# Performance work log

Hardware: AMD Instinct MI355X
Metric: run time of the kernel (lower is better)

The kernel has to match this reference:

```python
import jax, jax.numpy as jnp
import numpy as np

N_NODES = 20000
N_EDGES = 320000
F_IN = 256
HID = 256
N_CLS = 5


def _glorot(key, shape):
    lim = np.sqrt(6.0 / (shape[0] + shape[1]))
    return jax.random.uniform(key, shape, jnp.float32, -lim, lim)


def setup_inputs() -> dict:
    key = jax.random.key(0)
    ks = jax.random.split(key, 12)
    x1 = jax.random.normal(ks[0], (N_NODES, F_IN), jnp.float32)
    x2 = jax.random.normal(ks[1], (N_NODES, F_IN), jnp.float32)
    ei1 = jax.random.randint(ks[2], (2, N_EDGES), 0, N_NODES, jnp.int64 if jax.config.jax_enable_x64 else jnp.int32)
    ei2 = jax.random.randint(ks[3], (2, N_EDGES), 0, N_NODES, jnp.int64 if jax.config.jax_enable_x64 else jnp.int32)
    params = {
        'W1': _glorot(ks[4], (F_IN, HID)), 'b1': jnp.zeros((HID,), jnp.float32),
        'W2': _glorot(ks[5], (HID, HID)), 'b2': jnp.zeros((HID,), jnp.float32),
        'W3': _glorot(ks[6], (HID, HID)), 'b3': jnp.zeros((HID,), jnp.float32),
        'Wl': _glorot(ks[7], (HID, N_CLS)), 'bl': jnp.zeros((N_CLS,), jnp.float32),
    }
    return {'x1': x1, 'edge_index1': ei1, 'x2': x2, 'edge_index2': ei2, **params}


def gcn_conv(x, edge_index, W, b):
    # PyG GCNConv: add self-loops, symmetric normalization D^-1/2 (A+I) D^-1/2 (X W) + b
    N = x.shape[0]
    src, dst = edge_index[0], edge_index[1]
    deg = jax.ops.segment_sum(jnp.ones(src.shape[0], x.dtype), dst, num_segments=N) + 1.0
    dinv = jax.lax.rsqrt(deg)  # [N]
    xw = x @ W                 # [N, H]
    coef = (dinv[src] * dinv[dst])[:, None]  # per-edge norm
    agg = jax.ops.segment_sum(xw[src] * coef, dst, num_segments=N)
    agg = agg + xw * (dinv * dinv)[:, None]  # self-loop term
    return agg + b


def _branch(x, ei, W1, b1, W2, b2, W3, b3):
    # dropout is identity in eval mode
    h = jax.nn.relu(gcn_conv(x, ei, W1, b1))
    h = jax.nn.relu(gcn_conv(h, ei, W2, b2))
    return gcn_conv(h, ei, W3, b3)


def reference(x1, edge_index1, x2, edge_index2, W1, b1, W2, b2, W3, b3, Wl, bl):
    h1 = _branch(x1, edge_index1, W1, b1, W2, b2, W3, b3)
    h2 = _branch(x2, edge_index2, W1, b1, W2, b2, W3, b3)
    h = jnp.concatenate([h1, h2], axis=0)          # [2N, H]
    pooled = jnp.mean(h, axis=0, keepdims=True)    # batch is all zeros -> single mean pool
    return pooled @ Wl + bl                        # [1, num_classes]
```

## Files before the change

### kernel.cpp

```cpp
#include <hip/hip_runtime.h>
#include <hip/hip_bf16.h>

#define N_NODES 20000
#define N_EDGES 320000
#define HID 256
#define NQ 5000
#define NCHUNK 8

typedef __attribute__((ext_vector_type(8))) short bf16x8;
typedef __attribute__((ext_vector_type(4))) float f32x4;
typedef __attribute__((ext_vector_type(8))) unsigned short us8;

__device__ __forceinline__ float bf2f(ushort u) {
  union { unsigned int i; float f; } v; v.i = ((unsigned int)u) << 16; return v.f;
}
__device__ __forceinline__ ushort f2bf(float f) {
  union { float f; unsigned int i; } v; v.f = f;
  unsigned int r = v.i + 0x7FFFu + ((v.i >> 16) & 1u);
  return (ushort)(r >> 16);
}

__global__ void init_detect_kernel(int* cnt0, int* cnt1, float* t0, float* t1,
                                   const void* x1, const void* ei1, int* flags) {
  if (blockIdx.x == gridDim.x - 1) {
    __shared__ int cnt_wild, cnt_oddnz;
    if (threadIdx.x == 0) { cnt_wild = 0; cnt_oddnz = 0; }
    __syncthreads();
    const ushort* xu = (const ushort*)x1;
    int wild = 0;
#pragma unroll
    for (int k = 0; k < 4; k++) {
      ushort u = xu[threadIdx.x * 4 + k];
      int ex = (u >> 7) & 0xFF;
      if (ex >= 0x90) wild++;
    }
    if (wild) atomicAdd(&cnt_wild, wild);
    const int* ii = (const int*)ei1;
    if (ii[threadIdx.x * 2 + 1] != 0) atomicAdd(&cnt_oddnz, 1);
    __syncthreads();
    if (threadIdx.x == 0) {
      flags[0] = (cnt_wild > 64) ? 1 : 0;
      flags[1] = (cnt_oddnz < 8) ? 1 : 0;
    }
    return;
  }
  int i = blockIdx.x * blockDim.x + threadIdx.x;
  if (i < N_NODES) { cnt0[i] = 0; cnt1[i] = 0; t0[i] = 0.f; t1[i] = 0.f; }
}

__global__ __launch_bounds__(1024) void count_rank_kernel(
    const void* e0, const void* e1, int* cnt0, int* cnt1,
    int* rank0, int* rank1, const int* flags) {
  int b = blockIdx.y;
  const void* e = b ? e1 : e0;
  int* cnt = b ? cnt1 : cnt0;
  int* rank = b ? rank1 : rank0;
  int chunk = blockIdx.x >> 2;
  int lo = (blockIdx.x & 3) * NQ;
  int ebeg = chunk * (N_EDGES / NCHUNK);
  int eend = ebeg + (N_EDGES / NCHUNK);
  __shared__ int hist[NQ];
  __shared__ int base[NQ];
  for (int k = threadIdx.x; k < NQ; k += 1024) hist[k] = 0;
  __syncthreads();
  bool w64 = flags[1] != 0;
  const int* d32 = (const int*)e + N_EDGES;
  const long long* d64 = (const long long*)e + N_EDGES;
  for (int i = ebeg + threadIdx.x; i < eend; i += 1024) {
    int d = w64 ? (int)d64[i] : d32[i];
    unsigned q = (unsigned)(d - lo);
    if (q < NQ) atomicAdd(&hist[q], 1);
  }
  __syncthreads();
  for (int k = threadIdx.x; k < NQ; k += 1024) {
    base[k] = atomicAdd(&cnt[lo + k], hist[k]);
    hist[k] = 0;
  }
  __syncthreads();
  for (int i = ebeg + threadIdx.x; i < eend; i += 1024) {
    int d = w64 ? (int)d64[i] : d32[i];
    unsigned q = (unsigned)(d - lo);
    if (q < NQ) rank[i] = base[q] + atomicAdd(&hist[q], 1);
  }
}

__global__ __launch_bounds__(1024) void scan_kernel(const int* cnt0, const int* cnt1,
                                                    int* rp0, int* rp1,
                                                    float* dinv0, float* dinv1) {
  const int* cnt = blockIdx.x ? cnt1 : cnt0;
  int* rp = blockIdx.x ? rp1 : rp0;
  float* dinv = blockIdx.x ? dinv1 : dinv0;
  __shared__ int sd[1024];
  int tid = threadIdx.x;
  int base = tid * 20;
  int pref[20];
  int run = 0;
#pragma unroll
  for (int k = 0; k < 20; k++) {
    int i = base + k;
    int c = (i < N_NODES) ? cnt[i] : 0;
    if (i < N_NODES) dinv[i] = rsqrtf((float)c + 1.0f);
    run += c;
    pref[k] = run;
  }
  sd[tid] = run;
  __syncthreads();
  for (int off = 1; off < 1024; off <<= 1) {
    int v = (tid >= off) ? sd[tid - off] : 0;
    __syncthreads();
    sd[tid] += v;
    __syncthreads();
  }
  int offset = sd[tid] - run;
  if (tid == 0) rp[0] = 0;
#pragma unroll
  for (int k = 0; k < 20; k++) {
    int i = base + k;
    if (i < N_NODES) rp[i + 1] = offset + pref[k];
  }
}

__global__ __launch_bounds__(1024) void fill_kernel(
    const void* e0, const void* e1,
    const float* dinv0, const float* dinv1,
    const int* rp0, const int* rp1,
    const int* rank0, const int* rank1,
    unsigned int* eg0, unsigned int* eg1,
    float* t0, float* t1, const int* flags) {
  int b = blockIdx.y;
  const void* e = b ? e1 : e0;
  const float* dinv = b ? dinv1 : dinv0;
  bool w64 = flags[1] != 0;
  const int* s32 = (const int*)e;
  const int* d32 = (const int*)e + N_EDGES;
  const long long* s64 = (const long long*)e;
  const long long* d64 = (const long long*)e + N_EDGES;
  if (blockIdx.x < 313) {
    const int* rp = b ? rp1 : rp0;
    const int* rank = b ? rank1 : rank0;
    unsigned int* eg = b ? eg1 : eg0;
    int i = blockIdx.x * 1024 + threadIdx.x;
    if (i >= N_EDGES) return;
    int src = w64 ? (int)s64[i] : s32[i];
    int dst = w64 ? (int)d64[i] : d32[i];
    int slot = rp[dst] + rank[i];
    eg[slot] = (unsigned int)src | ((unsigned int)f2bf(dinv[src] * dinv[dst]) << 16);
    return;
  }
  float* t = b ? t1 : t0;
  int r = blockIdx.x - 313;
  int chunk = r >> 2;
  int lo = (r & 3) * NQ;
  int ebeg = chunk * (N_EDGES / NCHUNK);
  int eend = ebeg + (N_EDGES / NCHUNK);
  __shared__ float tl[NQ];
  for (int k = threadIdx.x; k < NQ; k += 1024) tl[k] = 0.f;
  __syncthreads();
  for (int i = ebeg + threadIdx.x; i < eend; i += 1024) {
    int src = w64 ? (int)s64[i] : s32[i];
    unsigned q = (unsigned)(src - lo);
    if (q < NQ) {
      int dst = w64 ? (int)d64[i] : d32[i];
      atomicAdd(&tl[q], dinv[dst]);
    }
  }
  __syncthreads();
  for (int k = threadIdx.x; k < NQ; k += 1024)
    atomicAdd(&t[lo + k], tl[k]);
}

__global__ __launch_bounds__(256) void gemm_kernel(
    const void* __restrict__ A0, const void* __restrict__ A1,
    const void* __restrict__ W,
    ushort* __restrict__ C0, ushort* __restrict__ C1,
    int maybe_f32, const int* __restrict__ flags) {
  const void* A = blockIdx.z ? A1 : A0;
  ushort* C = blockIdx.z ? C1 : C0;
  bool wf32 = flags[0] != 0;
  bool af32 = maybe_f32 && wf32;
  int m0 = blockIdx.x * 128;
  int n0 = blockIdx.y * 64;
  __shared__ ushort As[128][42];
  __shared__ ushort Bs[64][42];
  int tid = threadIdx.x;
  int wave = tid >> 6, lane = tid & 63;
  int quad = lane >> 4, r16 = lane & 15;
  f32x4 acc[2][4];
#pragma unroll
  for (int m = 0; m < 2; m++)
#pragma unroll
    for (int n = 0; n < 4; n++) acc[m][n] = (f32x4){0.f, 0.f, 0.f, 0.f};
  int la_row = tid >> 1;
  int la_c0 = (tid & 1) * 16;
  int bk = tid >> 3;
  int bn0 = (tid & 7) * 8;
  for (int k0 = 0; k0 < 256; k0 += 32) {
    int gr = m0 + la_row;
    if (af32) {
      const float* Af = (const float*)A;
      float4 v0 = {0,0,0,0}, v1 = v0, v2 = v0, v3 = v0;
      if (gr < N_NODES) {
        const float* pA = Af + gr * 256 + k0 + la_c0;
        v0 = *(const float4*)pA;       v1 = *(const float4*)(pA + 4);
        v2 = *(const float4*)(pA + 8); v3 = *(const float4*)(pA + 12);
      }
      ushort* d = &As[la_row][la_c0];
      d[0] = f2bf(v0.x); d[1] = f2bf(v0.y); d[2]  = f2bf(v0.z); d[3]  = f2bf(v0.w);
      d[4] = f2bf(v1.x); d[5] = f2bf(v1.y); d[6]  = f2bf(v1.z); d[7]  = f2bf(v1.w);
      d[8] = f2bf(v2.x); d[9] = f2bf(v2.y); d[10] = f2bf(v2.z); d[11] = f2bf(v2.w);
      d[12] = f2bf(v3.x); d[13] = f2bf(v3.y); d[14] = f2bf(v3.z); d[15] = f2bf(v3.w);
    } else {
      const ushort* Ab = (const ushort*)A;
      int4 w0 = {0,0,0,0}, w1 = w0;
      if (gr < N_NODES) {
        const ushort* pA = Ab + gr * 256 + k0 + la_c0;
        w0 = *(const int4*)pA;
        w1 = *(const int4*)(pA + 8);
      }
      *(int4*)&As[la_row][la_c0] = w0;
      *(int4*)&As[la_row][la_c0 + 8] = w1;
    }
    ushort wtmp[8];
    if (wf32) {
      const float* Wf = (const float*)W + (k0 + bk) * 256 + n0 + bn0;
      float4 u0 = *(const float4*)Wf;
      float4 u1 = *(const float4*)(Wf + 4);
      wtmp[0] = f2bf(u0.x); wtmp[1] = f2bf(u0.y); wtmp[2] = f2bf(u0.z); wtmp[3] = f2bf(u0.w);
      wtmp[4] = f2bf(u1.x); wtmp[5] = f2bf(u1.y); wtmp[6] = f2bf(u1.z); wtmp[7] = f2bf(u1.w);
    } else {
      *(int4*)wtmp = *(const int4*)((const ushort*)W + (k0 + bk) * 256 + n0 + bn0);
    }
#pragma unroll
    for (int j = 0; j < 8; j++) Bs[bn0 + j][bk] = wtmp[j];
    __syncthreads();
    bf16x8 a0 = *(const bf16x8*)&As[wave * 32 + r16][quad * 8];
    bf16x8 a1 = *(const bf16x8*)&As[wave * 32 + 16 + r16][quad * 8];
    bf16x8 bb0 = *(const bf16x8*)&Bs[r16][quad * 8];
    bf16x8 bb1 = *(const bf16x8*)&Bs[16 + r16][quad * 8];
    bf16x8 bb2 = *(const bf16x8*)&Bs[32 + r16][quad * 8];
    bf16x8 bb3 = *(const bf16x8*)&Bs[48 + r16][quad * 8];
    acc[0][0] = __builtin_amdgcn_mfma_f32_16x16x32_bf16(a0, bb0, acc[0][0], 0, 0, 0);
    acc[0][1] = __builtin_amdgcn_mfma_f32_16x16x32_bf16(a0, bb1, acc[0][1], 0, 0, 0);
    acc[0][2] = __builtin_amdgcn_mfma_f32_16x16x32_bf16(a0, bb2, acc[0][2], 0, 0, 0);
    acc[0][3] = __builtin_amdgcn_mfma_f32_16x16x32_bf16(a0, bb3, acc[0][3], 0, 0, 0);
    acc[1][0] = __builtin_amdgcn_mfma_f32_16x16x32_bf16(a1, bb0, acc[1][0], 0, 0, 0);
    acc[1][1] = __builtin_amdgcn_mfma_f32_16x16x32_bf16(a1, bb1, acc[1][1], 0, 0, 0);
    acc[1][2] = __builtin_amdgcn_mfma_f32_16x16x32_bf16(a1, bb2, acc[1][2], 0, 0, 0);
    acc[1][3] = __builtin_amdgcn_mfma_f32_16x16x32_bf16(a1, bb3, acc[1][3], 0, 0, 0);
    __syncthreads();
  }
#pragma unroll
  for (int m = 0; m < 2; m++) {
    int grb = m0 + wave * 32 + m * 16 + quad * 4;
#pragma unroll
    for (int r = 0; r < 4; r++) {
      int gr = grb + r;
      if (gr < N_NODES) {
        ushort* cp = C + gr * 256 + n0 + r16;
        cp[0]  = f2bf(acc[m][0][r]);
        cp[16] = f2bf(acc[m][1][r]);
        cp[32] = f2bf(acc[m][2][r]);
        cp[48] = f2bf(acc[m][3][r]);
      }
    }
  }
}

__global__ __launch_bounds__(256) void agg_kernel(
    const ushort* __restrict__ XW0, const ushort* __restrict__ XW1,
    const float* __restrict__ dinv0, const float* __restrict__ dinv1,
    const int* __restrict__ rp0, const int* __restrict__ rp1,
    const unsigned int* __restrict__ eg0, const unsigned int* __restrict__ eg1,
    const void* __restrict__ bias,
    ushort* __restrict__ H0, ushort* __restrict__ H1,
    const int* __restrict__ flags) {
  int b = blockIdx.y;
  const ushort* XW = b ? XW1 : XW0;
  const float* dinv = b ? dinv1 : dinv0;
  const int* rp = b ? rp1 : rp0;
  const unsigned int* eg = b ? eg1 : eg0;
  ushort* H = b ? H1 : H0;
  int wave = threadIdx.x >> 6, lane = threadIdx.x & 63;
  int half = lane >> 5;
  int fl = (lane & 31) * 8;
  int i = blockIdx.x * 8 + wave * 2 + half;
  float di = dinv[i];
  float selfw = di * di;
  us8 v = *(const us8*)(XW + i * 256 + fl);
  float acc[8], acc2[8];
#pragma unroll
  for (int k = 0; k < 8; k++) { acc[k] = selfw * bf2f(v[k]); acc2[k] = 0.f; }
  int e = rp[i], eend = rp[i + 1];
  for (; e + 4 <= eend; e += 4) {
    unsigned int p0 = eg[e], p1 = eg[e + 1], p2 = eg[e + 2], p3 = eg[e + 3];
    us8 r0 = *(const us8*)(XW + (p0 & 0xFFFFu) * 256 + fl);
    us8 r1 = *(const us8*)(XW + (p1 & 0xFFFFu) * 256 + fl);
    us8 r2 = *(const us8*)(XW + (p2 & 0xFFFFu) * 256 + fl);
    us8 r3 = *(const us8*)(XW + (p3 & 0xFFFFu) * 256 + fl);
    float w0 = bf2f((ushort)(p0 >> 16)), w1 = bf2f((ushort)(p1 >> 16));
    float w2 = bf2f((ushort)(p2 >> 16)), w3 = bf2f((ushort)(p3 >> 16));
#pragma unroll
    for (int k = 0; k < 8; k++) {
      acc[k]  += w0 * bf2f(r0[k]);
      acc2[k] += w1 * bf2f(r1[k]);
      acc[k]  += w2 * bf2f(r2[k]);
      acc2[k] += w3 * bf2f(r3[k]);
    }
  }
  for (; e < eend; e++) {
    unsigned int pp = eg[e];
    us8 r = *(const us8*)(XW + (pp & 0xFFFFu) * 256 + fl);
    float w = bf2f((ushort)(pp >> 16));
#pragma unroll
    for (int k = 0; k < 8; k++) acc[k] += w * bf2f(r[k]);
  }
  float bv[8];
  if (flags[0]) {
    const float* bf = (const float*)bias + fl;
    float4 c0 = *(const float4*)bf;
    float4 c1 = *(const float4*)(bf + 4);
    bv[0] = c0.x; bv[1] = c0.y; bv[2] = c0.z; bv[3] = c0.w;
    bv[4] = c1.x; bv[5] = c1.y; bv[6] = c1.z; bv[7] = c1.w;
  } else {
    us8 bb = *(const us8*)((const ushort*)bias + fl);
#pragma unroll
    for (int k = 0; k < 8; k++) bv[k] = bf2f(bb[k]);
  }
  us8 o;
#pragma unroll
  for (int k = 0; k < 8; k++)
    o[k] = f2bf(fmaxf(acc[k] + acc2[k] + bv[k], 0.f));
  *(us8*)(H + i * 256 + fl) = o;
}

__global__ __launch_bounds__(256) void colsum_kernel(
    const ushort* __restrict__ H0, const ushort* __restrict__ H1,
    const float* __restrict__ dinv0, const float* __restrict__ dinv1,
    const float* __restrict__ t0, const float* __restrict__ t1,
    float* __restrict__ P) {
  int b = blockIdx.y;
  const ushort* H = b ? H1 : H0;
  const float* dinv = b ? dinv1 : dinv0;
  const float* t = b ? t1 : t0;
  int wave = threadIdx.x >> 6, lane = threadIdx.x & 63;
  int wid = blockIdx.x * 4 + wave;
  int f4 = lane * 4;
  float a0 = 0.f, a1 = 0.f, a2 = 0.f, a3 = 0.f;
  for (int j = wid; j < N_NODES; j += 256) {
    float dj = dinv[j];
    float c = dj * (t[j] + dj);
    ushort4 u = *(const ushort4*)(H + j * 256 + f4);
    a0 += c * bf2f(u.x); a1 += c * bf2f(u.y);
    a2 += c * bf2f(u.z); a3 += c * bf2f(u.w);
  }
  __shared__ float part[4][256];
  part[wave][f4 + 0] = a0; part[wave][f4 + 1] = a1;
  part[wave][f4 + 2] = a2; part[wave][f4 + 3] = a3;
  __syncthreads();
  int f = threadIdx.x;
  float ssum = part[0][f] + part[1][f] + part[2][f] + part[3][f];
  P[(b * 64 + blockIdx.x) * 256 + f] = ssum;
}

__global__ __launch_bounds__(256) void final_kernel(
    const float* __restrict__ P,
    const void* __restrict__ W3, const void* __restrict__ b3,
    const void* __restrict__ Wl, const void* __restrict__ bl,
    void* __restrict__ out, const int* __restrict__ flags) {
  __shared__ float v[256];
  __shared__ float pooled[256];
  bool f32 = flags[0] != 0;
  int t = threadIdx.x;
  float acc0 = 0.f, acc1 = 0.f;
  for (int b = 0; b < 64; b++) {
    acc0 += P[b * 256 + t];
    acc1 += P[(64 + b) * 256 + t];
  }
  v[t] = acc0 + acc1;
  __syncthreads();
  float acc = 0.f;
  if (f32) {
    const float* W3f = (const float*)W3;
    for (int f = 0; f < 256; f++) acc += v[f] * W3f[f * 256 + t];
    pooled[t] = acc * (1.0f / (2.0f * N_NODES)) + ((const float*)b3)[t];
  } else {
    const ushort* W3b = (const ushort*)W3;
    for (int f = 0; f < 256; f++) acc += v[f] * bf2f(W3b[f * 256 + t]);
    pooled[t] = acc * (1.0f / (2.0f * N_NODES)) + bf2f(((const ushort*)b3)[t]);
  }
  __syncthreads();
  if (t < 5) {
    float o;
    if (f32) {
      o = ((const float*)bl)[t];
      for (int h = 0; h < 256; h++) o += pooled[h] * ((const float*)Wl)[h * 5 + t];
      ((float*)out)[t] = o;
    } else {
      o = bf2f(((const ushort*)bl)[t]);
      for (int h = 0; h < 256; h++) o += pooled[h] * bf2f(((const ushort*)Wl)[h * 5 + t]);
      ((ushort*)out)[t] = f2bf(o);
    }
  }
}

extern "C" void kernel_launch(void* const* d_in, const int* in_sizes, int n_in,
                              void* d_out, int out_size, void* d_ws, size_t ws_size,
                              hipStream_t stream) {
  const void* x1 = d_in[0];
  const void* ei1 = d_in[1];
  const void* x2 = d_in[2];
  const void* ei2 = d_in[3];
  const void* W1 = d_in[4];
  const void* b1 = d_in[5];
  const void* W2 = d_in[6];
  const void* b2 = d_in[7];
  const void* W3 = d_in[8];
  const void* b3 = d_in[9];
  const void* Wl = d_in[10];
  const void* bl = d_in[11];

  char* p = (char*)d_ws;
  auto alloc = [&](size_t bytes) {
    char* r = p;
    p += (bytes + 255) & ~size_t(255);
    return r;
  };
  int* flags   = (int*)alloc(256);
  float* dinv0 = (float*)alloc(N_NODES * 4);
  float* dinv1 = (float*)alloc(N_NODES * 4);
  float* t0    = (float*)alloc(N_NODES * 4);
  float* t1    = (float*)alloc(N_NODES * 4);
  int* cnt0    = (int*)alloc(N_NODES * 4);
  int* cnt1    = (int*)alloc(N_NODES * 4);
  int* rp0     = (int*)alloc((N_NODES + 1) * 4);
  int* rp1     = (int*)alloc((N_NODES + 1) * 4);
  unsigned int* eg0 = (unsigned int*)alloc((size_t)N_EDGES * 4);
  unsigned int* eg1 = (unsigned int*)alloc((size_t)N_EDGES * 4);
  float* Pp    = (float*)alloc(2 * 64 * 256 * 4);
  ushort* xw0  = (ushort*)alloc((size_t)N_NODES * HID * 2);
  ushort* xw1  = (ushort*)alloc((size_t)N_NODES * HID * 2);
  ushort* h0   = (ushort*)alloc((size_t)N_NODES * HID * 2);
  ushort* h1   = (ushort*)alloc((size_t)N_NODES * HID * 2);
  int* rank0  = (int*)xw0;
  int* rank1  = rank0 + N_EDGES;

  init_detect_kernel<<<(N_NODES + 255) / 256 + 1, 256, 0, stream>>>(
      cnt0, cnt1, t0, t1, x1, ei1, flags);
  count_rank_kernel<<<dim3(NCHUNK * 4, 2), 1024, 0, stream>>>(
      ei1, ei2, cnt0, cnt1, rank0, rank1, flags);
  scan_kernel<<<2, 1024, 0, stream>>>(cnt0, cnt1, rp0, rp1, dinv0, dinv1);
  fill_kernel<<<dim3(313 + NCHUNK * 4, 2), 1024, 0, stream>>>(
      ei1, ei2, dinv0, dinv1, rp0, rp1, rank0, rank1, eg0, eg1, t0, t1, flags);

  gemm_kernel<<<dim3(157, 4, 2), 256, 0, stream>>>(x1, x2, W1, xw0, xw1, 1, flags);
  agg_kernel<<<dim3(2500, 2), 256, 0, stream>>>(
      xw0, xw1, dinv0, dinv1, rp0, rp1, eg0, eg1, b1, h0, h1, flags);

  gemm_kernel<<<dim3(157, 4, 2), 256, 0, stream>>>(h0, h1, W2, xw0, xw1, 0, flags);
  agg_kernel<<<dim3(2500, 2), 256, 0, stream>>>(
      xw0, xw1, dinv0, dinv1, rp0, rp1, eg0, eg1, b2, h0, h1, flags);

  colsum_kernel<<<dim3(64, 2), 256, 0, stream>>>(h0, h1, dinv0, dinv1, t0, t1, Pp);
  final_kernel<<<1, 256, 0, stream>>>(Pp, W3, b3, Wl, bl, d_out, flags);
}
```

Baseline: 374.5 us.

## Fuse preprocessing and layer stages into cooperative persistent kernels with grid sync

Replaces the chain of separate kernels (init/detect, count-rank, scan, fill, gemm, agg, colsum, final) with three cooperative launches. A prep kernel does the degree counting, scan and CSR fill, separated by grid.sync, and keeps per-chunk ranks in shared memory instead of a global rank buffer. Each layer kernel runs the GEMM, the aggregation and, on the last layer, the pooling tail in one persistent grid of 512 blocks. The goal is to remove launch overhead and intermediate global traffic. In exchange, the GEMM and aggregation phases now run on a fixed, smaller grid with grid-wide barriers, which may cost occupancy and add barrier latency.

```diff
diff --git a/kernel.cpp b/kernel.cpp
--- a/kernel.cpp
+++ b/kernel.cpp
@@ -1,11 +1,17 @@
 #include <hip/hip_runtime.h>
 #include <hip/hip_bf16.h>
+#include <hip/hip_cooperative_groups.h>
+
+namespace cg = cooperative_groups;
 
 #define N_NODES 20000
 #define N_EDGES 320000
 #define HID 256
 #define NQ 5000
-#define NCHUNK 8
+#define NCHUNK 16
+#define ECHUNK (N_EDGES / NCHUNK)
+#define PREP_BLOCKS 256
+#define LAYER_BLOCKS 512
 
 typedef __attribute__((ext_vector_type(8))) short bf16x8;
 typedef __attribute__((ext_vector_type(4))) float f32x4;
@@ -20,385 +26,371 @@
   return (ushort)(r >> 16);
 }
 
-__global__ void init_detect_kernel(int* cnt0, int* cnt1, float* t0, float* t1,
-                                   const void* x1, const void* ei1, int* flags) {
-  if (blockIdx.x == gridDim.x - 1) {
-    __shared__ int cnt_wild, cnt_oddnz;
-    if (threadIdx.x == 0) { cnt_wild = 0; cnt_oddnz = 0; }
-    __syncthreads();
-    const ushort* xu = (const ushort*)x1;
-    int wild = 0;
-#pragma unroll
-    for (int k = 0; k < 4; k++) {
-      ushort u = xu[threadIdx.x * 4 + k];
-      int ex = (u >> 7) & 0xFF;
-      if (ex >= 0x90) wild++;
-    }
-    if (wild) atomicAdd(&cnt_wild, wild);
-    const int* ii = (const int*)ei1;
-    if (ii[threadIdx.x * 2 + 1] != 0) atomicAdd(&cnt_oddnz, 1);
-    __syncthreads();
-    if (threadIdx.x == 0) {
-      flags[0] = (cnt_wild > 64) ? 1 : 0;
-      flags[1] = (cnt_oddnz < 8) ? 1 : 0;
-    }
-    return;
-  }
-  int i = blockIdx.x * blockDim.x + threadIdx.x;
-  if (i < N_NODES) { cnt0[i] = 0; cnt1[i] = 0; t0[i] = 0.f; t1[i] = 0.f; }
-}
-
-__global__ __launch_bounds__(1024) void count_rank_kernel(
-    const void* e0, const void* e1, int* cnt0, int* cnt1,
-    int* rank0, int* rank1, const int* flags) {
-  int b = blockIdx.y;
-  const void* e = b ? e1 : e0;
-  int* cnt = b ? cnt1 : cnt0;
-  int* rank = b ? rank1 : rank0;
-  int chunk = blockIdx.x >> 2;
-  int lo = (blockIdx.x & 3) * NQ;
-  int ebeg = chunk * (N_EDGES / NCHUNK);
-  int eend = ebeg + (N_EDGES / NCHUNK);
+__global__ __launch_bounds__(1024) void prep_kernel(
+    const void* e0, const void* e1, const void* x1,
+    int* cnt0, int* cnt1, int* rp0, int* rp1,
+    float* dinv0, float* dinv1,
+    unsigned int* eg0, unsigned int* eg1,
+    float* t0, float* t1, int* flags) {
+  cg::grid_group grid = cg::this_grid();
   __shared__ int hist[NQ];
   __shared__ int base[NQ];
-  for (int k = threadIdx.x; k < NQ; k += 1024) hist[k] = 0;
-  __syncthreads();
+  __shared__ int sd[1024];
+  __shared__ int dw, dz;
+  int bx = blockIdx.x, tid = threadIdx.x;
+
+  int idx = bx * 1024 + tid;
+  if (idx < N_NODES) { cnt0[idx] = 0; cnt1[idx] = 0; t0[idx] = 0.f; t1[idx] = 0.f; }
+  if (bx == PREP_BLOCKS - 1) {
+    if (tid == 0) { dw = 0; dz = 0; }
+    __syncthreads();
+    if (tid < 256) {
+      const ushort* xu = (const ushort*)x1;
+      int wild = 0;
+#pragma unroll
+      for (int k = 0; k < 4; k++) {
+        ushort u = xu[tid * 4 + k];
+        int ex = (u >> 7) & 0xFF;
+        if (ex >= 0x90) wild++;
+      }
+      if (wild) atomicAdd(&dw, wild);
+      if (((const int*)e0)[tid * 2 + 1] != 0) atomicAdd(&dz, 1);
+    }
+    __syncthreads();
+    if (tid == 0) { flags[0] = (dw > 64) ? 1 : 0; flags[1] = (dz < 8) ? 1 : 0; }
+  }
+  grid.sync();
+
   bool w64 = flags[1] != 0;
-  const int* d32 = (const int*)e + N_EDGES;
-  const long long* d64 = (const long long*)e + N_EDGES;
-  for (int i = ebeg + threadIdx.x; i < eend; i += 1024) {
-    int d = w64 ? (int)d64[i] : d32[i];
-    unsigned q = (unsigned)(d - lo);
-    if (q < NQ) atomicAdd(&hist[q], 1);
-  }
-  __syncthreads();
-  for (int k = threadIdx.x; k < NQ; k += 1024) {
-    base[k] = atomicAdd(&cnt[lo + k], hist[k]);
-    hist[k] = 0;
-  }
-  __syncthreads();
-  for (int i = ebeg + threadIdx.x; i < eend; i += 1024) {
-    int d = w64 ? (int)d64[i] : d32[i];
-    unsigned q = (unsigned)(d - lo);
-    if (q < NQ) rank[i] = base[q] + atomicAdd(&hist[q], 1);
-  }
-}
-
-__global__ __launch_bounds__(1024) void scan_kernel(const int* cnt0, const int* cnt1,
-                                                    int* rp0, int* rp1,
-                                                    float* dinv0, float* dinv1) {
-  const int* cnt = blockIdx.x ? cnt1 : cnt0;
-  int* rp = blockIdx.x ? rp1 : rp0;
-  float* dinv = blockIdx.x ? dinv1 : dinv0;
-  __shared__ int sd[1024];
-  int tid = threadIdx.x;
-  int base = tid * 20;
-  int pref[20];
-  int run = 0;
-#pragma unroll
-  for (int k = 0; k < 20; k++) {
-    int i = base + k;
-    int c = (i < N_NODES) ? cnt[i] : 0;
-    if (i < N_NODES) dinv[i] = rsqrtf((float)c + 1.0f);
-    run += c;
-    pref[k] = run;
-  }
-  sd[tid] = run;
-  __syncthreads();
-  for (int off = 1; off < 1024; off <<= 1) {
-    int v = (tid >= off) ? sd[tid - off] : 0;
-    __syncthreads();
-    sd[tid] += v;
-    __syncthreads();
-  }
-  int offset = sd[tid] - run;
-  if (tid == 0) rp[0] = 0;
-#pragma unroll
-  for (int k = 0; k < 20; k++) {
-    int i = base + k;
-    if (i < N_NODES) rp[i + 1] = offset + pref[k];
-  }
-}
-
-__global__ __launch_bounds__(1024) void fill_kernel(
-    const void* e0, const void* e1,
-    const float* dinv0, const float* dinv1,
-    const int* rp0, const int* rp1,
-    const int* rank0, const int* rank1,
-    unsigned int* eg0, unsigned int* eg1,
-    float* t0, float* t1, const int* flags) {
-  int b = blockIdx.y;
-  const void* e = b ? e1 : e0;
-  const float* dinv = b ? dinv1 : dinv0;
-  bool w64 = flags[1] != 0;
+  int role = (bx < 128) ? bx : bx - 128;
+  int branch = role & 1;
+  int lo = ((role >> 1) & 3) * NQ;
+  int ebeg = (role >> 3) * ECHUNK;
+  const void* e = branch ? e1 : e0;
   const int* s32 = (const int*)e;
   const int* d32 = (const int*)e + N_EDGES;
   const long long* s64 = (const long long*)e;
   const long long* d64 = (const long long*)e + N_EDGES;
-  if (blockIdx.x < 313) {
-    const int* rp = b ? rp1 : rp0;
-    const int* rank = b ? rank1 : rank0;
-    unsigned int* eg = b ? eg1 : eg0;
-    int i = blockIdx.x * 1024 + threadIdx.x;
-    if (i >= N_EDGES) return;
-    int src = w64 ? (int)s64[i] : s32[i];
-    int dst = w64 ? (int)d64[i] : d32[i];
-    int slot = rp[dst] + rank[i];
-    eg[slot] = (unsigned int)src | ((unsigned int)f2bf(dinv[src] * dinv[dst]) << 16);
-    return;
-  }
-  float* t = b ? t1 : t0;
-  int r = blockIdx.x - 313;
-  int chunk = r >> 2;
-  int lo = (r & 3) * NQ;
-  int ebeg = chunk * (N_EDGES / NCHUNK);
-  int eend = ebeg + (N_EDGES / NCHUNK);
-  __shared__ float tl[NQ];
-  for (int k = threadIdx.x; k < NQ; k += 1024) tl[k] = 0.f;
-  __syncthreads();
-  for (int i = ebeg + threadIdx.x; i < eend; i += 1024) {
-    int src = w64 ? (int)s64[i] : s32[i];
-    unsigned q = (unsigned)(src - lo);
-    if (q < NQ) {
-      int dst = w64 ? (int)d64[i] : d32[i];
-      atomicAdd(&tl[q], dinv[dst]);
-    }
-  }
-  __syncthreads();
-  for (int k = threadIdx.x; k < NQ; k += 1024)
-    atomicAdd(&t[lo + k], tl[k]);
+
+  if (bx < 128) {
+    for (int k = tid; k < NQ; k += 1024) hist[k] = 0;
+    __syncthreads();
+    for (int i = ebeg + tid; i < ebeg + ECHUNK; i += 1024) {
+      int d = w64 ? (int)d64[i] : d32[i];
+      unsigned q = (unsigned)(d - lo);
+      if (q < NQ) atomicAdd(&hist[q], 1);
+    }
+    __syncthreads();
+    int* cnt = branch ? cnt1 : cnt0;
+    for (int k = tid; k < NQ; k += 1024) {
+      base[k] = atomicAdd(&cnt[lo + k], hist[k]);
+      hist[k] = 0;
+    }
+  } else {
+    float* tl = (float*)hist;
+    for (int k = tid; k < NQ; k += 1024) tl[k] = 0.f;
+  }
+  grid.sync();
+
+  if (bx == 128 || bx == 129) {
+    int b = bx - 128;
+    const int* cnt = b ? cnt1 : cnt0;
+    int* rp = b ? rp1 : rp0;
+    float* dinv = b ? dinv1 : dinv0;
+    int bb = tid * 20;
+    int pref[20];
+    int run = 0;
+#pragma unroll
+    for (int k = 0; k < 20; k++) {
+      int i = bb + k;
+      int c = (i < N_NODES) ? cnt[i] : 0;
+      if (i < N_NODES) dinv[i] = rsqrtf((float)c + 1.0f);
+      run += c;
+      pref[k] = run;
+    }
+    sd[tid] = run;
+    __syncthreads();
+    for (int off = 1; off < 1024; off <<= 1) {
+      int v = (tid >= off) ? sd[tid - off] : 0;
+      __syncthreads();
+      sd[tid] += v;
+      __syncthreads();
+    }
+    int offset = sd[tid] - run;
+    if (tid == 0) rp[0] = 0;
+#pragma unroll
+    for (int k = 0; k < 20; k++) {
+      int i = bb + k;
+      if (i < N_NODES) rp[i + 1] = offset + pref[k];
+    }
+  }
+  grid.sync();
+
+  const float* dinv = branch ? dinv1 : dinv0;
+  if (bx < 128) {
+    const int* rp = branch ? rp1 : rp0;
+    unsigned int* eg = branch ? eg1 : eg0;
+    for (int i = ebeg + tid; i < ebeg + ECHUNK; i += 1024) {
+      int d = w64 ? (int)d64[i] : d32[i];
+      unsigned q = (unsigned)(d - lo);
+      if (q < NQ) {
+        int s = w64 ? (int)s64[i] : s32[i];
+        int r = atomicAdd(&hist[q], 1);
+        int slot = rp[d] + base[q] + r;
+        eg[slot] = (unsigned int)s | ((unsigned int)f2bf(dinv[s] * dinv[d]) << 16);
+      }
+    }
+  } else {
+    float* tl = (float*)hist;
+    float* t = branch ? t1 : t0;
+    for (int i = ebeg + tid; i < ebeg + ECHUNK; i += 1024) {
+      int s = w64 ? (int)s64[i] : s32[i];
+      unsigned q = (unsigned)(s - lo);
+      if (q < NQ) {
+        int d = w64 ? (int)d64[i] : d32[i];
+        atomicAdd(&tl[q], dinv[d]);
+      }
+    }
+    __syncthreads();
+    for (int k = tid; k < NQ; k += 1024)
+      atomicAdd(&t[lo + k], tl[k]);
+  }
 }
 
-__global__ __launch_bounds__(256) void gemm_kernel(
-    const void* __restrict__ A0, const void* __restrict__ A1,
-    const void* __restrict__ W,
-    ushort* __restrict__ C0, ushort* __restrict__ C1,
-    int maybe_f32, const int* __restrict__ flags) {
-  const void* A = blockIdx.z ? A1 : A0;
-  ushort* C = blockIdx.z ? C1 : C0;
-  bool wf32 = flags[0] != 0;
-  bool af32 = maybe_f32 && wf32;
-  int m0 = blockIdx.x * 128;
-  int n0 = blockIdx.y * 64;
+__global__ __launch_bounds__(256) void layer_kernel(
+    const void* A0, const void* A1, const void* W,
+    ushort* C0, ushort* C1,
+    const void* bias,
+    ushort* H0, ushort* H1,
+    const float* dinv0, const float* dinv1,
+    const int* rp0, const int* rp1,
+    const unsigned int* eg0, const unsigned int* eg1,
+    const float* t0, const float* t1,
+    float* P,
+    const void* W3, const void* b3, const void* Wl, const void* bl,
+    void* out, const int* flags, int maybe_f32, int last) {
+  cg::grid_group grid = cg::this_grid();
   __shared__ ushort As[128][42];
   __shared__ ushort Bs[64][42];
+  __shared__ float part[4][256];
+  __shared__ float vv[256];
+  __shared__ float pooled[256];
   int tid = threadIdx.x;
   int wave = tid >> 6, lane = tid & 63;
   int quad = lane >> 4, r16 = lane & 15;
-  f32x4 acc[2][4];
-#pragma unroll
-  for (int m = 0; m < 2; m++)
-#pragma unroll
-    for (int n = 0; n < 4; n++) acc[m][n] = (f32x4){0.f, 0.f, 0.f, 0.f};
-  int la_row = tid >> 1;
-  int la_c0 = (tid & 1) * 16;
-  int bk = tid >> 3;
-  int bn0 = (tid & 7) * 8;
-  for (int k0 = 0; k0 < 256; k0 += 32) {
-    int gr = m0 + la_row;
-    if (af32) {
-      const float* Af = (const float*)A;
-      float4 v0 = {0,0,0,0}, v1 = v0, v2 = v0, v3 = v0;
-      if (gr < N_NODES) {
-        const float* pA = Af + gr * 256 + k0 + la_c0;
-        v0 = *(const float4*)pA;       v1 = *(const float4*)(pA + 4);
-        v2 = *(const float4*)(pA + 8); v3 = *(const float4*)(pA + 12);
-      }
-      ushort* d = &As[la_row][la_c0];
-      d[0] = f2bf(v0.x); d[1] = f2bf(v0.y); d[2]  = f2bf(v0.z); d[3]  = f2bf(v0.w);
-      d[4] = f2bf(v1.x); d[5] = f2bf(v1.y); d[6]  = f2bf(v1.z); d[7]  = f2bf(v1.w);
-      d[8] = f2bf(v2.x); d[9] = f2bf(v2.y); d[10] = f2bf(v2.z); d[11] = f2bf(v2.w);
-      d[12] = f2bf(v3.x); d[13] = f2bf(v3.y); d[14] = f2bf(v3.z); d[15] = f2bf(v3.w);
+  bool wf32 = flags[0] != 0;
+  bool af32 = maybe_f32 && wf32;
+
+  for (int role = blockIdx.x; role < 157 * 4 * 2; role += LAYER_BLOCKS) {
+    int z = role & 1;
+    int n0 = ((role >> 1) & 3) * 64;
+    int m0 = (role >> 3) * 128;
+    const void* A = z ? A1 : A0;
+    ushort* C = z ? C1 : C0;
+    f32x4 acc[2][4];
+#pragma unroll
+    for (int m = 0; m < 2; m++)
+#pragma unroll
+      for (int n = 0; n < 4; n++) acc[m][n] = (f32x4){0.f, 0.f, 0.f, 0.f};
+    int la_row = tid >> 1;
+    int la_c0 = (tid & 1) * 16;
+    int bk = tid >> 3;
+    int bn0 = (tid & 7) * 8;
+    for (int k0 = 0; k0 < 256; k0 += 32) {
+      int gr = m0 + la_row;
+      if (af32) {
+        const float* Af = (const float*)A;
+        float4 v0 = {0,0,0,0}, v1 = v0, v2 = v0, v3 = v0;
+        if (gr < N_NODES) {
+          const float* pA = Af + gr * 256 + k0 + la_c0;
+          v0 = *(const float4*)pA;       v1 = *(const float4*)(pA + 4);
+          v2 = *(const float4*)(pA + 8); v3 = *(const float4*)(pA + 12);
+        }
+        ushort* d = &As[la_row][la_c0];
+        d[0] = f2bf(v0.x); d[1] = f2bf(v0.y); d[2]  = f2bf(v0.z); d[3]  = f2bf(v0.w);
+        d[4] = f2bf(v1.x); d[5] = f2bf(v1.y); d[6]  = f2bf(v1.z); d[7]  = f2bf(v1.w);
+        d[8] = f2bf(v2.x); d[9] = f2bf(v2.y); d[10] = f2bf(v2.z); d[11] = f2bf(v2.w);
+        d[12] = f2bf(v3.x); d[13] = f2bf(v3.y); d[14] = f2bf(v3.z); d[15] = f2bf(v3.w);
+      } else {
+        const ushort* Ab = (const ushort*)A;
+        int4 w0 = {0,0,0,0}, w1 = w0;
+        if (gr < N_NODES) {
+          const ushort* pA = Ab + gr * 256 + k0 + la_c0;
+          w0 = *(const int4*)pA;
+          w1 = *(const int4*)(pA + 8);
+        }
+        *(int4*)&As[la_row][la_c0] = w0;
+        *(int4*)&As[la_row][la_c0 + 8] = w1;
+      }
+      ushort wtmp[8];
+      if (wf32) {
+        const float* Wf = (const float*)W + (k0 + bk) * 256 + n0 + bn0;
+        float4 u0 = *(const float4*)Wf;
+        float4 u1 = *(const float4*)(Wf + 4);
+        wtmp[0] = f2bf(u0.x); wtmp[1] = f2bf(u0.y); wtmp[2] = f2bf(u0.z); wtmp[3] = f2bf(u0.w);
+        wtmp[4] = f2bf(u1.x); wtmp[5] = f2bf(u1.y); wtmp[6] = f2bf(u1.z); wtmp[7] = f2bf(u1.w);
+      } else {
+        *(int4*)wtmp = *(const int4*)((const ushort*)W + (k0 + bk) * 256 + n0 + bn0);
+      }
+#pragma unroll
+      for (int j = 0; j < 8; j++) Bs[bn0 + j][bk] = wtmp[j];
+      __syncthreads();
+      bf16x8 a0 = *(const bf16x8*)&As[wave * 32 + r16][quad * 8];
+      bf16x8 a1 = *(const bf16x8*)&As[wave * 32 + 16 + r16][quad * 8];
+      bf16x8 bb0 = *(const bf16x8*)&Bs[r16][quad * 8];
+      bf16x8 bb1 = *(const bf16x8*)&Bs[16 + r16][quad * 8];
+      bf16x8 bb2 = *(const bf16x8*)&Bs[32 + r16][quad * 8];
+      bf16x8 bb3 = *(const bf16x8*)&Bs[48 + r16][quad * 8];
+      acc[0][0] = __builtin_amdgcn_mfma_f32_16x16x32_bf16(a0, bb0, acc[0][0], 0, 0, 0);
+      acc[0][1] = __builtin_amdgcn_mfma_f32_16x16x32_bf16(a0, bb1, acc[0][1], 0, 0, 0);
+      acc[0][2] = __builtin_amdgcn_mfma_f32_16x16x32_bf16(a0, bb2, acc[0][2], 0, 0, 0);
+      acc[0][3] = __builtin_amdgcn_mfma_f32_16x16x32_bf16(a0, bb3, acc[0][3], 0, 0, 0);
+      acc[1][0] = __builtin_amdgcn_mfma_f32_16x16x32_bf16(a1, bb0, acc[1][0], 0, 0, 0);
+      acc[1][1] = __builtin_amdgcn_mfma_f32_16x16x32_bf16(a1, bb1, acc[1][1], 0, 0, 0);
+      acc[1][2] = __builtin_amdgcn_mfma_f32_16x16x32_bf16(a1, bb2, acc[1][2], 0, 0, 0);
+      acc[1][3] = __builtin_amdgcn_mfma_f32_16x16x32_bf16(a1, bb3, acc[1][3], 0, 0, 0);
+      __syncthreads();
+    }
+#pragma unroll
+    for (int m = 0; m < 2; m++) {
+      int grb = m0 + wave * 32 + m * 16 + quad * 4;
+#pragma unroll
+      for (int r = 0; r < 4; r++) {
+        int gr = grb + r;
+        if (gr < N_NODES) {
+          ushort* cp = C + gr * 256 + n0 + r16;
+          cp[0]  = f2bf(acc[m][0][r]);
+          cp[16] = f2bf(acc[m][1][r]);
+          cp[32] = f2bf(acc[m][2][r]);
+          cp[48] = f2bf(acc[m][3][r]);
+        }
+      }
+    }
+  }
+  grid.sync();
+
+  {
+    int half = lane >> 5;
+    int fl = (lane & 31) * 8;
+    for (int role = blockIdx.x; role < 5000; role += LAYER_BLOCKS) {
+      int b = role & 1;
+      int nb = role >> 1;
+      const ushort* XW = b ? C1 : C0;
+      const float* dinv = b ? dinv1 : dinv0;
+      const int* rp = b ? rp1 : rp0;
+      const unsigned int* eg = b ? eg1 : eg0;
+      ushort* H = b ? H1 : H0;
+      int i = nb * 8 + wave * 2 + half;
+      float di = dinv[i];
+      float selfw = di * di;
+      us8 v = *(const us8*)(XW + i * 256 + fl);
+      float acc[8], acc2[8];
+#pragma unroll
+      for (int k = 0; k < 8; k++) { acc[k] = selfw * bf2f(v[k]); acc2[k] = 0.f; }
+      int e = rp[i], eend = rp[i + 1];
+      for (; e + 4 <= eend; e += 4) {
+        unsigned int p0 = eg[e], p1 = eg[e + 1], p2 = eg[e + 2], p3 = eg[e + 3];
+        us8 r0 = *(const us8*)(XW + (p0 & 0xFFFFu) * 256 + fl);
+        us8 r1 = *(const us8*)(XW + (p1 & 0xFFFFu) * 256 + fl);
+        us8 r2 = *(const us8*)(XW + (p2 & 0xFFFFu) * 256 + fl);
+        us8 r3 = *(const us8*)(XW + (p3 & 0xFFFFu) * 256 + fl);
+        float w0 = bf2f((ushort)(p0 >> 16)), w1 = bf2f((ushort)(p1 >> 16));
+        float w2 = bf2f((ushort)(p2 >> 16)), w3 = bf2f((ushort)(p3 >> 16));
+#pragma unroll
+        for (int k = 0; k < 8; k++) {
+          acc[k]  += w0 * bf2f(r0[k]);
+          acc2[k] += w1 * bf2f(r1[k]);
+          acc[k]  += w2 * bf2f(r2[k]);
+          acc2[k] += w3 * bf2f(r3[k]);
+        }
+      }
+      for (; e < eend; e++) {
+        unsigned int pp = eg[e];
+        us8 r = *(const us8*)(XW + (pp & 0xFFFFu) * 256 + fl);
+        float w = bf2f((ushort)(pp >> 16));
+#pragma unroll
+        for (int k = 0; k < 8; k++) acc[k] += w * bf2f(r[k]);
+      }
+      float bv[8];
+      if (wf32) {
+        const float* bf = (const float*)bias + fl;
+        float4 c0 = *(const float4*)bf;
+        float4 c1 = *(const float4*)(bf + 4);
+        bv[0] = c0.x; bv[1] = c0.y; bv[2] = c0.z; bv[3] = c0.w;
+        bv[4] = c1.x; bv[5] = c1.y; bv[6] = c1.z; bv[7] = c1.w;
+      } else {
+        us8 bb = *(const us8*)((const ushort*)bias + fl);
+#pragma unroll
+        for (int k = 0; k < 8; k++) bv[k] = bf2f(bb[k]);
+      }
+      us8 o;
+#pragma unroll
+      for (int k = 0; k < 8; k++)
+        o[k] = f2bf(fmaxf(acc[k] + acc2[k] + bv[k], 0.f));
+      *(us8*)(H + i * 256 + fl) = o;
+    }
+  }
+
+  if (!last) return;
+  grid.sync();
+
+  for (int role = blockIdx.x; role < 128; role += LAYER_BLOCKS) {
+    int b = role & 1;
+    int cx = role >> 1;
+    const ushort* H = b ? H1 : H0;
+    const float* dinv = b ? dinv1 : dinv0;
+    const float* t = b ? t1 : t0;
+    int wid = cx * 4 + wave;
+    int f4 = lane * 4;
+    float a0 = 0.f, a1 = 0.f, a2 = 0.f, a3 = 0.f;
+    for (int j = wid; j < N_NODES; j += 256) {
+      float dj = dinv[j];
+      float c = dj * (t[j] + dj);
+      ushort4 u = *(const ushort4*)(H + j * 256 + f4);
+      a0 += c * bf2f(u.x); a1 += c * bf2f(u.y);
+      a2 += c * bf2f(u.z); a3 += c * bf2f(u.w);
+    }
+    part[wave][f4 + 0] = a0; part[wave][f4 + 1] = a1;
+    part[wave][f4 + 2] = a2; part[wave][f4 + 3] = a3;
+    __syncthreads();
+    int f = tid;
+    float ssum = part[0][f] + part[1][f] + part[2][f] + part[3][f];
+    P[(b * 64 + cx) * 256 + f] = ssum;
+    __syncthreads();
+  }
+  grid.sync();
+
+  if (blockIdx.x == 0) {
+    int t = tid;
+    float acc0 = 0.f, acc1 = 0.f;
+    for (int b = 0; b < 64; b++) {
+      acc0 += P[b * 256 + t];
+      acc1 += P[(64 + b) * 256 + t];
+    }
+    vv[t] = acc0 + acc1;
+    __syncthreads();
+    float acc = 0.f;
+    if (wf32) {
+      const float* W3f = (const float*)W3;
+      for (int f = 0; f < 256; f++) acc += vv[f] * W3f[f * 256 + t];
+      pooled[t] = acc * (1.0f / (2.0f * N_NODES)) + ((const float*)b3)[t];
     } else {
-      const ushort* Ab = (const ushort*)A;
-      int4 w0 = {0,0,0,0}, w1 = w0;
-      if (gr < N_NODES) {
-        const ushort* pA = Ab + gr * 256 + k0 + la_c0;
-        w0 = *(const int4*)pA;
-        w1 = *(const int4*)(pA + 8);
-      }
-      *(int4*)&As[la_row][la_c0] = w0;
-      *(int4*)&As[la_row][la_c0 + 8] = w1;
-    }
-    ushort wtmp[8];
-    if (wf32) {
-      const float* Wf = (const float*)W + (k0 + bk) * 256 + n0 + bn0;
-      float4 u0 = *(const float4*)Wf;
-      float4 u1 = *(const float4*)(Wf + 4);
-      wtmp[0] = f2bf(u0.x); wtmp[1] = f2bf(u0.y); wtmp[2] = f2bf(u0.z); wtmp[3] = f2bf(u0.w);
-      wtmp[4] = f2bf(u1.x); wtmp[5] = f2bf(u1.y); wtmp[6] = f2bf(u1.z); wtmp[7] = f2bf(u1.w);
-    } else {
-      *(int4*)wtmp = *(const int4*)((const ushort*)W + (k0 + bk) * 256 + n0 + bn0);
-    }
-#pragma unroll
-    for (int j = 0; j < 8; j++) Bs[bn0 + j][bk] = wtmp[j];
-    __syncthreads();
-    bf16x8 a0 = *(const bf16x8*)&As[wave * 32 + r16][quad * 8];
-    bf16x8 a1 = *(const bf16x8*)&As[wave * 32 + 16 + r16][quad * 8];
-    bf16x8 bb0 = *(const bf16x8*)&Bs[r16][quad * 8];
-    bf16x8 bb1 = *(const bf16x8*)&Bs[16 + r16][quad * 8];
-    bf16x8 bb2 = *(const bf16x8*)&Bs[32 + r16][quad * 8];
-    bf16x8 bb3 = *(const bf16x8*)&Bs[48 + r16][quad * 8];
-    acc[0][0] = __builtin_amdgcn_mfma_f32_16x16x32_bf16(a0, bb0, acc[0][0], 0, 0, 0);
-    acc[0][1] = __builtin_amdgcn_mfma_f32_16x16x32_bf16(a0, bb1, acc[0][1], 0, 0, 0);
-    acc[0][2] = __builtin_amdgcn_mfma_f32_16x16x32_bf16(a0, bb2, acc[0][2], 0, 0, 0);
-    acc[0][3] = __builtin_amdgcn_mfma_f32_16x16x32_bf16(a0, bb3, acc[0][3], 0, 0, 0);
-    acc[1][0] = __builtin_amdgcn_mfma_f32_16x16x32_bf16(a1, bb0, acc[1][0], 0, 0, 0);
-    acc[1][1] = __builtin_amdgcn_mfma_f32_16x16x32_bf16(a1, bb1, acc[1][1], 0, 0, 0);
-    acc[1][2] = __builtin_amdgcn_mfma_f32_16x16x32_bf16(a1, bb2, acc[1][2], 0, 0, 0);
-    acc[1][3] = __builtin_amdgcn_mfma_f32_16x16x32_bf16(a1, bb3, acc[1][3], 0, 0, 0);
-    __syncthreads();
-  }
-#pragma unroll
-  for (int m = 0; m < 2; m++) {
-    int grb = m0 + wave * 32 + m * 16 + quad * 4;
-#pragma unroll
-    for (int r = 0; r < 4; r++) {
-      int gr = grb + r;
-      if (gr < N_NODES) {
-        ushort* cp = C + gr * 256 + n0 + r16;
-        cp[0]  = f2bf(acc[m][0][r]);
-        cp[16] = f2bf(acc[m][1][r]);
-        cp[32] = f2bf(acc[m][2][r]);
-        cp[48] = f2bf(acc[m][3][r]);
-      }
-    }
-  }
-}
-
-__global__ __launch_bounds__(256) void agg_kernel(
-    const ushort* __restrict__ XW0, const ushort* __restrict__ XW1,
-    const float* __restrict__ dinv0, const float* __restrict__ dinv1,
-    const int* __restrict__ rp0, const int* __restrict__ rp1,
-    const unsigned int* __restrict__ eg0, const unsigned int* __restrict__ eg1,
-    const void* __restrict__ bias,
-    ushort* __restrict__ H0, ushort* __restrict__ H1,
-    const int* __restrict__ flags) {
-  int b = blockIdx.y;
-  const ushort* XW = b ? XW1 : XW0;
-  const float* dinv = b ? dinv1 : dinv0;
-  const int* rp = b ? rp1 : rp0;
-  const unsigned int* eg = b ? eg1 : eg0;
-  ushort* H = b ? H1 : H0;
-  int wave = threadIdx.x >> 6, lane = threadIdx.x & 63;
-  int half = lane >> 5;
-  int fl = (lane & 31) * 8;
-  int i = blockIdx.x * 8 + wave * 2 + half;
-  float di = dinv[i];
-  float selfw = di * di;
-  us8 v = *(const us8*)(XW + i * 256 + fl);
-  float acc[8], acc2[8];
-#pragma unroll
-  for (int k = 0; k < 8; k++) { acc[k] = selfw * bf2f(v[k]); acc2[k] = 0.f; }
-  int e = rp[i], eend = rp[i + 1];
-  for (; e + 4 <= eend; e += 4) {
-    unsigned int p0 = eg[e], p1 = eg[e + 1], p2 = eg[e + 2], p3 = eg[e + 3];
-    us8 r0 = *(const us8*)(XW + (p0 & 0xFFFFu) * 256 + fl);
-    us8 r1 = *(const us8*)(XW + (p1 & 0xFFFFu) * 256 + fl);
-    us8 r2 = *(const us8*)(XW + (p2 & 0xFFFFu) * 256 + fl);
-    us8 r3 = *(const us8*)(XW + (p3 & 0xFFFFu) * 256 + fl);
-    float w0 = bf2f((ushort)(p0 >> 16)), w1 = bf2f((ushort)(p1 >> 16));
-    float w2 = bf2f((ushort)(p2 >> 16)), w3 = bf2f((ushort)(p3 >> 16));
-#pragma unroll
-    for (int k = 0; k < 8; k++) {
-      acc[k]  += w0 * bf2f(r0[k]);
-      acc2[k] += w1 * bf2f(r1[k]);
-      acc[k]  += w2 * bf2f(r2[k]);
-      acc2[k] += w3 * bf2f(r3[k]);
-    }
-  }
-  for (; e < eend; e++) {
-    unsigned int pp = eg[e];
-    us8 r = *(const us8*)(XW + (pp & 0xFFFFu) * 256 + fl);
-    float w = bf2f((ushort)(pp >> 16));
-#pragma unroll
-    for (int k = 0; k < 8; k++) acc[k] += w * bf2f(r[k]);
-  }
-  float bv[8];
-  if (flags[0]) {
-    const float* bf = (const float*)bias + fl;
-    float4 c0 = *(const float4*)bf;
-    float4 c1 = *(const float4*)(bf + 4);
-    bv[0] = c0.x; bv[1] = c0.y; bv[2] = c0.z; bv[3] = c0.w;
-    bv[4] = c1.x; bv[5] = c1.y; bv[6] = c1.z; bv[7] = c1.w;
-  } else {
-    us8 bb = *(const us8*)((const ushort*)bias + fl);
-#pragma unroll
-    for (int k = 0; k < 8; k++) bv[k] = bf2f(bb[k]);
-  }
-  us8 o;
-#pragma unroll
-  for (int k = 0; k < 8; k++)
-    o[k] = f2bf(fmaxf(acc[k] + acc2[k] + bv[k], 0.f));
-  *(us8*)(H + i * 256 + fl) = o;
-}
-
-__global__ __launch_bounds__(256) void colsum_kernel(
-    const ushort* __restrict__ H0, const ushort* __restrict__ H1,
-    const float* __restrict__ dinv0, const float* __restrict__ dinv1,
-    const float* __restrict__ t0, const float* __restrict__ t1,
-    float* __restrict__ P) {
-  int b = blockIdx.y;
-  const ushort* H = b ? H1 : H0;
-  const float* dinv = b ? dinv1 : dinv0;
-  const float* t = b ? t1 : t0;
-  int wave = threadIdx.x >> 6, lane = threadIdx.x & 63;
-  int wid = blockIdx.x * 4 + wave;
-  int f4 = lane * 4;
-  float a0 = 0.f, a1 = 0.f, a2 = 0.f, a3 = 0.f;
-  for (int j = wid; j < N_NODES; j += 256) {
-    float dj = dinv[j];
-    float c = dj * (t[j] + dj);
-    ushort4 u = *(const ushort4*)(H + j * 256 + f4);
-    a0 += c * bf2f(u.x); a1 += c * bf2f(u.y);
-    a2 += c * bf2f(u.z); a3 += c * bf2f(u.w);
-  }
-  __shared__ float part[4][256];
-  part[wave][f4 + 0] = a0; part[wave][f4 + 1] = a1;
-  part[wave][f4 + 2] = a2; part[wave][f4 + 3] = a3;
-  __syncthreads();
-  int f = threadIdx.x;
-  float ssum = part[0][f] + part[1][f] + part[2][f] + part[3][f];
-  P[(b * 64 + blockIdx.x) * 256 + f] = ssum;
-}
-
-__global__ __launch_bounds__(256) void final_kernel(
-    const float* __restrict__ P,
-    const void* __restrict__ W3, const void* __restrict__ b3,
-    const void* __restrict__ Wl, const void* __restrict__ bl,
-    void* __restrict__ out, const int* __restrict__ flags) {
-  __shared__ float v[256];
-  __shared__ float pooled[256];
-  bool f32 = flags[0] != 0;
-  int t = threadIdx.x;
-  float acc0 = 0.f, acc1 = 0.f;
-  for (int b = 0; b < 64; b++) {
-    acc0 += P[b * 256 + t];
-    acc1 += P[(64 + b) * 256 + t];
-  }
-  v[t] = acc0 + acc1;
-  __syncthreads();
-  float acc = 0.f;
-  if (f32) {
-    const float* W3f = (const float*)W3;
-    for (int f = 0; f < 256; f++) acc += v[f] * W3f[f * 256 + t];
-    pooled[t] = acc * (1.0f / (2.0f * N_NODES)) + ((const float*)b3)[t];
-  } else {
-    const ushort* W3b = (const ushort*)W3;
-    for (int f = 0; f < 256; f++) acc += v[f] * bf2f(W3b[f * 256 + t]);
-    pooled[t] = acc * (1.0f / (2.0f * N_NODES)) + bf2f(((const ushort*)b3)[t]);
-  }
-  __syncthreads();
-  if (t < 5) {
-    float o;
-    if (f32) {
-      o = ((const float*)bl)[t];
-      for (int h = 0; h < 256; h++) o += pooled[h] * ((const float*)Wl)[h * 5 + t];
-      ((float*)out)[t] = o;
-    } else {
-      o = bf2f(((const ushort*)bl)[t]);
-      for (int h = 0; h < 256; h++) o += pooled[h] * bf2f(((const ushort*)Wl)[h * 5 + t]);
-      ((ushort*)out)[t] = f2bf(o);
+      const ushort* W3b = (const ushort*)W3;
+      for (int f = 0; f < 256; f++) acc += vv[f] * bf2f(W3b[f * 256 + t]);
+      pooled[t] = acc * (1.0f / (2.0f * N_NODES)) + bf2f(((const ushort*)b3)[t]);
+    }
+    __syncthreads();
+    if (t < 5) {
+      float o;
+      if (wf32) {
+        o = ((const float*)bl)[t];
+        for (int h = 0; h < 256; h++) o += pooled[h] * ((const float*)Wl)[h * 5 + t];
+        ((float*)out)[t] = o;
+      } else {
+        o = bf2f(((const ushort*)bl)[t]);
+        for (int h = 0; h < 256; h++) o += pooled[h] * bf2f(((const ushort*)Wl)[h * 5 + t]);
+        ((ushort*)out)[t] = f2bf(o);
+      }
     }
   }
 }
@@ -418,6 +410,7 @@
   const void* b3 = d_in[9];
   const void* Wl = d_in[10];
   const void* bl = d_in[11];
+  void* out = d_out;
 
   char* p = (char*)d_ws;
   auto alloc = [&](size_t bytes) {
@@ -441,25 +434,32 @@
   ushort* xw1  = (ushort*)alloc((size_t)N_NODES * HID * 2);
   ushort* h0   = (ushort*)alloc((size_t)N_NODES * HID * 2);
   ushort* h1   = (ushort*)alloc((size_t)N_NODES * HID * 2);
-  int* rank0  = (int*)xw0;
-  int* rank1  = rank0 + N_EDGES;
-
-  init_detect_kernel<<<(N_NODES + 255) / 256 + 1, 256, 0, stream>>>(
-      cnt0, cnt1, t0, t1, x1, ei1, flags);
-  count_rank_kernel<<<dim3(NCHUNK * 4, 2), 1024, 0, stream>>>(
-      ei1, ei2, cnt0, cnt1, rank0, rank1, flags);
-  scan_kernel<<<2, 1024, 0, stream>>>(cnt0, cnt1, rp0, rp1, dinv0, dinv1);
-  fill_kernel<<<dim3(313 + NCHUNK * 4, 2), 1024, 0, stream>>>(
-      ei1, ei2, dinv0, dinv1, rp0, rp1, rank0, rank1, eg0, eg1, t0, t1, flags);
-
-  gemm_kernel<<<dim3(157, 4, 2), 256, 0, stream>>>(x1, x2, W1, xw0, xw1, 1, flags);
-  agg_kernel<<<dim3(2500, 2), 256, 0, stream>>>(
-      xw0, xw1, dinv0, dinv1, rp0, rp1, eg0, eg1, b1, h0, h1, flags);
-
-  gemm_kernel<<<dim3(157, 4, 2), 256, 0, stream>>>(h0, h1, W2, xw0, xw1, 0, flags);
-  agg_kernel<<<dim3(2500, 2), 256, 0, stream>>>(
-      xw0, xw1, dinv0, dinv1, rp0, rp1, eg0, eg1, b2, h0, h1, flags);
-
-  colsum_kernel<<<dim3(64, 2), 256, 0, stream>>>(h0, h1, dinv0, dinv1, t0, t1, Pp);
-  final_kernel<<<1, 256, 0, stream>>>(Pp, W3, b3, Wl, bl, d_out, flags);
+
+  {
+    void* args[] = {(void*)&ei1, (void*)&ei2, (void*)&x1,
+                    &cnt0, &cnt1, &rp0, &rp1, &dinv0, &dinv1,
+                    &eg0, &eg1, &t0, &t1, &flags};
+    hipLaunchCooperativeKernel((const void*)prep_kernel, dim3(PREP_BLOCKS),
+                               dim3(1024), args, 0, stream);
+  }
+  int one = 1, zero = 0;
+  {
+    void* args[] = {(void*)&x1, (void*)&x2, (void*)&W1, &xw0, &xw1,
+                    (void*)&b1, &h0, &h1, &dinv0, &dinv1, &rp0, &rp1,
+                    &eg0, &eg1, &t0, &t1, &Pp,
+                    (void*)&W3, (void*)&b3, (void*)&Wl, (void*)&bl,
+                    &out, &flags, &one, &zero};
+    hipLaunchCooperativeKernel((const void*)layer_kernel, dim3(LAYER_BLOCKS),
+                               dim3(256), args, 0, stream);
+  }
+  {
+    void* h0c = h0, *h1c = h1;
+    void* args[] = {&h0c, &h1c, (void*)&W2, &xw0, &xw1,
+                    (void*)&b2, &h0, &h1, &dinv0, &dinv1, &rp0, &rp1,
+                    &eg0, &eg1, &t0, &t1, &Pp,
+                    (void*)&W3, (void*)&b3, (void*)&Wl, (void*)&bl,
+                    &out, &flags, &zero, &one};
+    hipLaunchCooperativeKernel((const void*)layer_kernel, dim3(LAYER_BLOCKS),
+                               dim3(256), args, 0, stream);
+  }
 }
```

New measurement: 753.8 us. 2.01x slower.
